# Performance work log

Measured on AMD Instinct MI355X. Metric: run time of the kernel, lower is better.

Reference implementation:

```python
import jax, jax.numpy as jnp
import numpy as np

T, K, E, H, I = 1024, 2, 8, 2048, 1024


def setup_inputs() -> dict:
    key = jax.random.key(0)
    k1, k2, k3, k4 = jax.random.split(key, 4)
    hidden_states = jax.random.normal(k1, (T, H), dtype=jnp.float32)
    selected_experts = jax.random.randint(k2, (T, K), 0, E, dtype=jnp.int32)
    # glorot-ish scale for the batched expert kernels
    gu_scale = (2.0 / (H + 2 * I)) ** 0.5
    dn_scale = (2.0 / (I + H)) ** 0.5
    gate_up_proj = jax.random.normal(k3, (E, 2 * I, H), dtype=jnp.float32) * gu_scale
    down_proj = jax.random.normal(k4, (E, H, I), dtype=jnp.float32) * dn_scale
    return {
        "hidden_states": hidden_states,
        "selected_experts": selected_experts,
        "gate_up_proj": gate_up_proj,
        "down_proj": down_proj,
    }


def reference(hidden_states, selected_experts, gate_up_proj, down_proj):
    # Mathematically identical to the original per-token weight gather
    # (ops.take + 'th,temh->tem'), but expressed as dense all-expert GEMMs
    # followed by an output gather, avoiding the T*k*2I*H weight blowup.
    # gate_up_all: (T, E, 2I)
    gate_up_all = jnp.einsum("th,emh->tem", hidden_states, gate_up_proj)
    gate, up = jnp.split(gate_up_all, 2, axis=-1)
    intermediate = jax.nn.silu(gate) * up                # (T, E, I)
    out_all = jnp.einsum("tem,ehm->teh", intermediate, down_proj)  # (T, E, H)
    # select the top-k experts' outputs per token -> (T, K, H)
    return jnp.take_along_axis(out_all, selected_experts[..., None].astype(jnp.int32), axis=1)
```

## Files before the change

kernel.cpp:

```cpp
#include <hip/hip_runtime.h>
#include <hip/hip_bf16.h>

#define T_TOK 1024
#define KSEL  2
#define NEXP  8
#define HDIM  2048
#define IDIM  1024
#define TK    (T_TOK * KSEL)

#define RS 40

typedef float  f32x4  __attribute__((ext_vector_type(4)));
typedef __bf16 bf16x8 __attribute__((ext_vector_type(8)));
typedef __bf16 bf16x2 __attribute__((ext_vector_type(2)));

__device__ __forceinline__ unsigned short f2bf(float f) {
    union { float f; unsigned u; } v; v.f = f;
    unsigned r = (v.u >> 16) & 1u;
    return (unsigned short)((v.u + 0x7fffu + r) >> 16);
}

__device__ __forceinline__ unsigned pk2bf(float lo, float hi) {
#if __has_builtin(__builtin_amdgcn_cvt_pk_bf16_f32)
    bf16x2 v = __builtin_amdgcn_cvt_pk_bf16_f32(lo, hi);
    union { bf16x2 v; unsigned u; } c; c.v = v;
    return c.u;
#else
    return (unsigned)f2bf(lo) | ((unsigned)f2bf(hi) << 16);
#endif
}

__device__ __forceinline__ void st_bf4(unsigned short* dst, float4 v) {
    uint2 u;
    u.x = pk2bf(v.x, v.y);
    u.y = pk2bf(v.z, v.w);
    *(uint2*)dst = u;
}

__global__ void build_pairs(const int* __restrict__ sel, int* __restrict__ meta,
                            int* __restrict__ pairs) {
    __shared__ int lcnt[NEXP], lstart[NEXP], lfill[NEXP];
    const int tid = threadIdx.x;
    if (tid < NEXP) { lcnt[tid] = 0; lfill[tid] = 0; }
    __syncthreads();
    for (int idx = tid; idx < TK; idx += 256) atomicAdd(&lcnt[sel[idx]], 1);
    __syncthreads();
    if (tid == 0) {
        int s = 0;
        for (int e = 0; e < NEXP; ++e) { lstart[e] = s; s += lcnt[e]; }
    }
    __syncthreads();
    for (int idx = tid; idx < TK; idx += 256) {
        int e = sel[idx];
        int pos = lstart[e] + atomicAdd(&lfill[e], 1);
        pairs[pos] = idx;
    }
    if (tid < NEXP) { meta[tid] = lcnt[tid]; meta[NEXP + tid] = lstart[tid]; }
}

__global__ __launch_bounds__(256) void gemm1_gateup(
    const float* __restrict__ hidden, const float* __restrict__ gup,
    const int* __restrict__ meta, const int* __restrict__ pairs,
    unsigned short* __restrict__ inter)
{
    __shared__ __align__(16) unsigned short As[2][64 * RS];
    __shared__ __align__(16) unsigned short Bs[2][128 * RS];

    const int bx = blockIdx.x;
    const int nt = bx & 15, e = (bx >> 4) & 7, mt = bx >> 7;
    const int cnt = meta[e];
    const int m0 = mt * 64;
    if (m0 >= cnt) return;
    const int seg  = meta[8 + e];
    const int rows = min(64, cnt - m0);
    const int n0   = nt * 64;

    const int tid  = threadIdx.x;
    const int lane = tid & 63, wave = tid >> 6;
    const int quad = lane >> 4, l16 = lane & 15;
    const int wm = wave >> 1, wn = wave & 1;

    const float* __restrict__ Wb = gup + (size_t)e * (2 * IDIM * HDIM);

    const float* aptr[2]; bool aval[2]; int aofs[2];
    #pragma unroll
    for (int c = 0; c < 2; ++c) {
        int id = tid + c * 256;
        int r = id >> 3, col = (id & 7) * 4;
        aval[c] = (r < rows);
        int tok = aval[c] ? (pairs[seg + m0 + r] >> 1) : 0;
        aptr[c] = hidden + (size_t)tok * HDIM + col;
        aofs[c] = r * RS + col;
    }
    const float* bptr[4]; int bofs[4];
    #pragma unroll
    for (int c = 0; c < 4; ++c) {
        int id = tid + c * 256;
        int r = id >> 3, col = (id & 7) * 4;
        int wr = (r < 64) ? (n0 + r) : (IDIM + n0 + (r - 64));
        bptr[c] = Wb + (size_t)wr * HDIM + col;
        bofs[c] = r * RS + col;
    }

    f32x4 accg[2][2], accu[2][2];
    const f32x4 zero = {0.f, 0.f, 0.f, 0.f};
    #pragma unroll
    for (int i = 0; i < 2; ++i)
        #pragma unroll
        for (int j = 0; j < 2; ++j) { accg[i][j] = zero; accu[i][j] = zero; }

    const float4 z4 = make_float4(0.f, 0.f, 0.f, 0.f);
    float4 Qa0[2], Qb0[4], Qa1[2], Qb1[4];

    auto load0 = [&](int k0) {
        #pragma unroll
        for (int c = 0; c < 2; ++c) Qa0[c] = aval[c] ? *(const float4*)(aptr[c] + k0) : z4;
        #pragma unroll
        for (int c = 0; c < 4; ++c) Qb0[c] = *(const float4*)(bptr[c] + k0);
    };
    auto load1 = [&](int k0) {
        #pragma unroll
        for (int c = 0; c < 2; ++c) Qa1[c] = aval[c] ? *(const float4*)(aptr[c] + k0) : z4;
        #pragma unroll
        for (int c = 0; c < 4; ++c) Qb1[c] = *(const float4*)(bptr[c] + k0);
    };
    auto store0 = [&](int buf) {
        #pragma unroll
        for (int c = 0; c < 2; ++c) st_bf4(&As[buf][aofs[c]], Qa0[c]);
        #pragma unroll
        for (int c = 0; c < 4; ++c) st_bf4(&Bs[buf][bofs[c]], Qb0[c]);
    };
    auto store1 = [&](int buf) {
        #pragma unroll
        for (int c = 0; c < 2; ++c) st_bf4(&As[buf][aofs[c]], Qa1[c]);
        #pragma unroll
        for (int c = 0; c < 4; ++c) st_bf4(&Bs[buf][bofs[c]], Qb1[c]);
    };
    auto compute = [&](int buf) {
        bf16x8 af[2], bg[2], bu[2];
        const int kq = quad * 8;
        #pragma unroll
        for (int i = 0; i < 2; ++i)
            af[i] = *(const bf16x8*)&As[buf][(wm * 32 + i * 16 + l16) * RS + kq];
        #pragma unroll
        for (int j = 0; j < 2; ++j) {
            bg[j] = *(const bf16x8*)&Bs[buf][(wn * 32 + j * 16 + l16) * RS + kq];
            bu[j] = *(const bf16x8*)&Bs[buf][(64 + wn * 32 + j * 16 + l16) * RS + kq];
        }
        #pragma unroll
        for (int i = 0; i < 2; ++i)
            #pragma unroll
            for (int j = 0; j < 2; ++j) {
                accg[i][j] = __builtin_amdgcn_mfma_f32_16x16x32_bf16(af[i], bg[j], accg[i][j], 0, 0, 0);
                accu[i][j] = __builtin_amdgcn_mfma_f32_16x16x32_bf16(af[i], bu[j], accu[i][j], 0, 0, 0);
            }
    };

    const int NK = HDIM / 32;
    load0(0);
    store0(0);
    load1(32);
    load0(64);
    __syncthreads();

    for (int k = 0; ; k += 2) {
        compute(0);
        store1(1);
        if (k + 3 < NK) load1((k + 3) * 32);
        __syncthreads();
        compute(1);
        if (k + 2 >= NK) break;
        store0(0);
        if (k + 4 < NK) load0((k + 4) * 32);
        __syncthreads();
    }

    #pragma unroll
    for (int i = 0; i < 2; ++i) {
        #pragma unroll
        for (int r = 0; r < 4; ++r) {
            int ml = wm * 32 + i * 16 + quad * 4 + r;
            if (ml < rows) {
                size_t orow = (size_t)(seg + m0 + ml) * IDIM;
                #pragma unroll
                for (int j = 0; j < 2; ++j) {
                    int n = n0 + wn * 32 + j * 16 + l16;
                    float g = accg[i][j][r], u = accu[i][j][r];
                    float s = g * (1.f / (1.f + __expf(-g)));
                    inter[orow + n] = f2bf(s * u);
                }
            }
        }
    }
}

__global__ __launch_bounds__(256, 4) void gemm2_down(
    const unsigned short* __restrict__ inter, const float* __restrict__ down,
    const int* __restrict__ meta, const int* __restrict__ pairs,
    float* __restrict__ out)
{
    __shared__ __align__(16) unsigned short As[2][64 * RS];
    __shared__ __align__(16) unsigned short Bs[2][64 * RS];

    const int bx = blockIdx.x;
    const int nt = bx & 31, e = (bx >> 5) & 7, mt = bx >> 8;
    const int cnt = meta[e];
    const int m0 = mt * 64;
    if (m0 >= cnt) return;
    const int seg  = meta[8 + e];
    const int rows = min(64, cnt - m0);
    const int n0   = nt * 64;

    const int tid  = threadIdx.x;
    const int lane = tid & 63, wave = tid >> 6;
    const int quad = lane >> 4, l16 = lane & 15;
    const int wm = wave >> 1, wn = wave & 1;

    const float* __restrict__ Db = down + (size_t)e * (HDIM * IDIM);

    const int ar = tid >> 2, ako = (tid & 3) * 8;
    const bool aval = (ar < rows);
    const unsigned short* iptr = inter + (size_t)(seg + m0 + (aval ? ar : 0)) * IDIM + ako;
    const int aofs = ar * RS + ako;

    const float* bptr[2]; int bofs[2];
    #pragma unroll
    for (int c = 0; c < 2; ++c) {
        int id = tid + c * 256;
        int r = id >> 3, col = (id & 7) * 4;
        bptr[c] = Db + (size_t)(n0 + r) * IDIM + col;
        bofs[c] = r * RS + col;
    }

    f32x4 acc[2][2];
    const f32x4 zero = {0.f, 0.f, 0.f, 0.f};
    #pragma unroll
    for (int i = 0; i < 2; ++i)
        #pragma unroll
        for (int j = 0; j < 2; ++j) acc[i][j] = zero;

    const uint4 zu4 = make_uint4(0u, 0u, 0u, 0u);
    uint4 QaU0, QaU1; float4 Qb0[2], Qb1[2];

    auto load0 = [&](int k0) {
        QaU0 = aval ? *(const uint4*)(iptr + k0) : zu4;
        #pragma unroll
        for (int c = 0; c < 2; ++c) Qb0[c] = *(const float4*)(bptr[c] + k0);
    };
    auto load1 = [&](int k0) {
        QaU1 = aval ? *(const uint4*)(iptr + k0) : zu4;
        #pragma unroll
        for (int c = 0; c < 2; ++c) Qb1[c] = *(const float4*)(bptr[c] + k0);
    };
    auto store0 = [&](int buf) {
        *(uint4*)&As[buf][aofs] = QaU0;
        #pragma unroll
        for (int c = 0; c < 2; ++c) st_bf4(&Bs[buf][bofs[c]], Qb0[c]);
    };
    auto store1 = [&](int buf) {
        *(uint4*)&As[buf][aofs] = QaU1;
        #pragma unroll
        for (int c = 0; c < 2; ++c) st_bf4(&Bs[buf][bofs[c]], Qb1[c]);
    };
    auto compute = [&](int buf) {
        bf16x8 af[2], bf[2];
        const int kq = quad * 8;
        #pragma unroll
        for (int i = 0; i < 2; ++i)
            af[i] = *(const bf16x8*)&As[buf][(wm * 32 + i * 16 + l16) * RS + kq];
        #pragma unroll
        for (int j = 0; j < 2; ++j)
            bf[j] = *(const bf16x8*)&Bs[buf][(wn * 32 + j * 16 + l16) * RS + kq];
        #pragma unroll
        for (int i = 0; i < 2; ++i)
            #pragma unroll
            for (int j = 0; j < 2; ++j)
                acc[i][j] = __builtin_amdgcn_mfma_f32_16x16x32_bf16(af[i], bf[j], acc[i][j], 0, 0, 0);
    };

    const int NK = IDIM / 32;
    load0(0);
    store0(0);
    load1(32);
    load0(64);
    __syncthreads();

    for (int k = 0; ; k += 2) {
        compute(0);
        store1(1);
        if (k + 3 < NK) load1((k + 3) * 32);
        __syncthreads();
        compute(1);
        if (k + 2 >= NK) break;
        store0(0);
        if (k + 4 < NK) load0((k + 4) * 32);
        __syncthreads();
    }

    #pragma unroll
    for (int i = 0; i < 2; ++i) {
        #pragma unroll
        for (int r = 0; r < 4; ++r) {
            int ml = wm * 32 + i * 16 + quad * 4 + r;
            if (ml < rows) {
                int p = pairs[seg + m0 + ml];
                size_t ob = (size_t)p * HDIM + n0 + wn * 32 + l16;
                #pragma unroll
                for (int j = 0; j < 2; ++j)
                    out[ob + j * 16] = acc[i][j][r];
            }
        }
    }
}

extern "C" void kernel_launch(void* const* d_in, const int* in_sizes, int n_in,
                              void* d_out, int out_size, void* d_ws, size_t ws_size,
                              hipStream_t stream) {
    const float* hidden = (const float*)d_in[0];
    const int*   sel    = (const int*)  d_in[1];
    const float* gup    = (const float*)d_in[2];
    const float* down   = (const float*)d_in[3];
    float* out = (float*)d_out;

    int* meta  = (int*)d_ws;
    int* pairs = meta + 16;
    unsigned short* inter = (unsigned short*)((char*)d_ws + 16384);

    build_pairs<<<1, 256, 0, stream>>>(sel, meta, pairs);
    gemm1_gateup<<<4096, 256, 0, stream>>>(hidden, gup, meta, pairs, inter);
    gemm2_down  <<<8192, 256, 0, stream>>>(inter, down, meta, pairs, out);
}
```

Measured before the change: 339.0 us.

## Pre-convert weights and activations to bf16 and widen K tile to 64

```diff
diff --git a/kernel.cpp b/kernel.cpp
--- a/kernel.cpp
+++ b/kernel.cpp
@@ -8,7 +8,8 @@
 #define IDIM  1024
 #define TK    (T_TOK * KSEL)
 
-#define RS 40
+#define BK 64
+#define RS 72
 
 typedef float  f32x4  __attribute__((ext_vector_type(4)));
 typedef __bf16 bf16x8 __attribute__((ext_vector_type(8)));
@@ -30,13 +31,6 @@
 #endif
 }
 
-__device__ __forceinline__ void st_bf4(unsigned short* dst, float4 v) {
-    uint2 u;
-    u.x = pk2bf(v.x, v.y);
-    u.y = pk2bf(v.z, v.w);
-    *(uint2*)dst = u;
-}
-
 __global__ void build_pairs(const int* __restrict__ sel, int* __restrict__ meta,
                             int* __restrict__ pairs) {
     __shared__ int lcnt[NEXP], lstart[NEXP], lfill[NEXP];
@@ -58,16 +52,159 @@
     if (tid < NEXP) { meta[tid] = lcnt[tid]; meta[NEXP + tid] = lstart[tid]; }
 }
 
-__global__ __launch_bounds__(256) void gemm1_gateup(
-    const float* __restrict__ hidden, const float* __restrict__ gup,
+__global__ __launch_bounds__(256) void cvt_all(
+    const float* __restrict__ gup, const float* __restrict__ down,
+    const float* __restrict__ hidden, unsigned short* __restrict__ gup_bf,
+    unsigned short* __restrict__ down_bf, unsigned short* __restrict__ hid_bf)
+{
+    const long NG = (long)NEXP * 2 * IDIM * HDIM / 8;
+    const long ND = (long)NEXP * HDIM * IDIM / 8;
+    const long NH = (long)T_TOK * HDIM / 8;
+    const long NT = NG + ND + NH;
+    for (long i = (long)blockIdx.x * 256 + threadIdx.x; i < NT;
+         i += (long)gridDim.x * 256) {
+        const float* s; unsigned short* d; long c;
+        if (i < NG)           { s = gup;    d = gup_bf;  c = i; }
+        else if (i < NG + ND) { s = down;   d = down_bf; c = i - NG; }
+        else                  { s = hidden; d = hid_bf;  c = i - NG - ND; }
+        float4 v0 = *(const float4*)(s + c * 8);
+        float4 v1 = *(const float4*)(s + c * 8 + 4);
+        uint4 o;
+        o.x = pk2bf(v0.x, v0.y); o.y = pk2bf(v0.z, v0.w);
+        o.z = pk2bf(v1.x, v1.y); o.w = pk2bf(v1.z, v1.w);
+        *(uint4*)(d + c * 8) = o;
+    }
+}
+
+__global__ __launch_bounds__(256, 4) void gemm1_gateup(
+    const unsigned short* __restrict__ hid_bf, const unsigned short* __restrict__ gup_bf,
     const int* __restrict__ meta, const int* __restrict__ pairs,
     unsigned short* __restrict__ inter)
 {
     __shared__ __align__(16) unsigned short As[2][64 * RS];
-    __shared__ __align__(16) unsigned short Bs[2][128 * RS];
+    __shared__ __align__(16) unsigned short Bs[2][64 * RS];
 
     const int bx = blockIdx.x;
-    const int nt = bx & 15, e = (bx >> 4) & 7, mt = bx >> 7;
+    const int e = bx & 7, mt = (bx >> 3) & 31, nt = bx >> 8;
+    const int cnt = meta[e];
+    const int m0 = mt * 64;
+    if (m0 >= cnt) return;
+    const int seg  = meta[8 + e];
+    const int rows = min(64, cnt - m0);
+    const int n0   = nt * 32;
+
+    const int tid  = threadIdx.x;
+    const int lane = tid & 63, wave = tid >> 6;
+    const int quad = lane >> 4, l16 = lane & 15;
+    const int wm = wave >> 1, wn = wave & 1;
+
+    const unsigned short* __restrict__ Wb = gup_bf + (size_t)e * (2 * IDIM * HDIM);
+
+    const unsigned short* aptr[2]; int aofs[2];
+    #pragma unroll
+    for (int c = 0; c < 2; ++c) {
+        int id = tid + c * 256;
+        int row = id >> 3, kc = (id & 7) * 8;
+        int ar = min(row, rows - 1);
+        int tok = pairs[seg + m0 + ar] >> 1;
+        aptr[c] = hid_bf + (size_t)tok * HDIM + kc;
+        aofs[c] = row * RS + kc;
+    }
+    const unsigned short* bptr[2]; int bofs[2];
+    #pragma unroll
+    for (int c = 0; c < 2; ++c) {
+        int id = tid + c * 256;
+        int row = id >> 3, kc = (id & 7) * 8;
+        int gr = (row < 32) ? (n0 + row) : (IDIM + n0 + (row - 32));
+        bptr[c] = Wb + (size_t)gr * HDIM + kc;
+        bofs[c] = row * RS + kc;
+    }
+
+    f32x4 accg[2], accu[2];
+    const f32x4 zero = {0.f, 0.f, 0.f, 0.f};
+    accg[0] = zero; accg[1] = zero; accu[0] = zero; accu[1] = zero;
+
+    uint4 Qa0[2], Qb0[2], Qa1[2], Qb1[2];
+    auto load0 = [&](int k0) {
+        #pragma unroll
+        for (int c = 0; c < 2; ++c) { Qa0[c] = *(const uint4*)(aptr[c] + k0);
+                                      Qb0[c] = *(const uint4*)(bptr[c] + k0); }
+    };
+    auto load1 = [&](int k0) {
+        #pragma unroll
+        for (int c = 0; c < 2; ++c) { Qa1[c] = *(const uint4*)(aptr[c] + k0);
+                                      Qb1[c] = *(const uint4*)(bptr[c] + k0); }
+    };
+    auto store0 = [&](int buf) {
+        #pragma unroll
+        for (int c = 0; c < 2; ++c) { *(uint4*)&As[buf][aofs[c]] = Qa0[c];
+                                      *(uint4*)&Bs[buf][bofs[c]] = Qb0[c]; }
+    };
+    auto store1 = [&](int buf) {
+        #pragma unroll
+        for (int c = 0; c < 2; ++c) { *(uint4*)&As[buf][aofs[c]] = Qa1[c];
+                                      *(uint4*)&Bs[buf][bofs[c]] = Qb1[c]; }
+    };
+    auto compute = [&](int buf) {
+        #pragma unroll
+        for (int ks = 0; ks < 2; ++ks) {
+            const int kq = ks * 32 + quad * 8;
+            bf16x8 af0 = *(const bf16x8*)&As[buf][(wm * 32 + l16) * RS + kq];
+            bf16x8 af1 = *(const bf16x8*)&As[buf][(wm * 32 + 16 + l16) * RS + kq];
+            bf16x8 bg  = *(const bf16x8*)&Bs[buf][(wn * 16 + l16) * RS + kq];
+            bf16x8 bu  = *(const bf16x8*)&Bs[buf][(32 + wn * 16 + l16) * RS + kq];
+            accg[0] = __builtin_amdgcn_mfma_f32_16x16x32_bf16(af0, bg, accg[0], 0, 0, 0);
+            accg[1] = __builtin_amdgcn_mfma_f32_16x16x32_bf16(af1, bg, accg[1], 0, 0, 0);
+            accu[0] = __builtin_amdgcn_mfma_f32_16x16x32_bf16(af0, bu, accu[0], 0, 0, 0);
+            accu[1] = __builtin_amdgcn_mfma_f32_16x16x32_bf16(af1, bu, accu[1], 0, 0, 0);
+        }
+    };
+
+    const int NK = HDIM / BK;
+    load0(0);
+    store0(0);
+    load1(BK);
+    load0(2 * BK);
+    __syncthreads();
+    for (int k = 0; ; k += 2) {
+        compute(0);
+        store1(1);
+        if (k + 3 < NK) load1((k + 3) * BK);
+        __syncthreads();
+        compute(1);
+        if (k + 2 >= NK) break;
+        store0(0);
+        if (k + 4 < NK) load0((k + 4) * BK);
+        __syncthreads();
+    }
+
+    #pragma unroll
+    for (int i = 0; i < 2; ++i) {
+        #pragma unroll
+        for (int r = 0; r < 4; ++r) {
+            int ml = wm * 32 + i * 16 + quad * 4 + r;
+            if (ml < rows) {
+                size_t orow = (size_t)(seg + m0 + ml) * IDIM;
+                int n = n0 + wn * 16 + l16;
+                float g = (i == 0) ? accg[0][r] : accg[1][r];
+                float u = (i == 0) ? accu[0][r] : accu[1][r];
+                float s = g * (1.f / (1.f + __expf(-g)));
+                inter[orow + n] = f2bf(s * u);
+            }
+        }
+    }
+}
+
+__global__ __launch_bounds__(256, 4) void gemm2_down(
+    const unsigned short* __restrict__ inter, const unsigned short* __restrict__ down_bf,
+    const int* __restrict__ meta, const int* __restrict__ pairs,
+    float* __restrict__ out)
+{
+    __shared__ __align__(16) unsigned short As[2][64 * RS];
+    __shared__ __align__(16) unsigned short Bs[2][64 * RS];
+
+    const int bx = blockIdx.x;
+    const int e = bx & 7, mt = (bx >> 3) & 31, nt = bx >> 8;
     const int cnt = meta[e];
     const int m0 = mt * 64;
     if (m0 >= cnt) return;
@@ -80,220 +217,81 @@
     const int quad = lane >> 4, l16 = lane & 15;
     const int wm = wave >> 1, wn = wave & 1;
 
-    const float* __restrict__ Wb = gup + (size_t)e * (2 * IDIM * HDIM);
-
-    const float* aptr[2]; bool aval[2]; int aofs[2];
+    const unsigned short* __restrict__ Db = down_bf + (size_t)e * (HDIM * IDIM);
+
+    const unsigned short* aptr[2]; int aofs[2];
     #pragma unroll
     for (int c = 0; c < 2; ++c) {
         int id = tid + c * 256;
-        int r = id >> 3, col = (id & 7) * 4;
-        aval[c] = (r < rows);
-        int tok = aval[c] ? (pairs[seg + m0 + r] >> 1) : 0;
-        aptr[c] = hidden + (size_t)tok * HDIM + col;
-        aofs[c] = r * RS + col;
-    }
-    const float* bptr[4]; int bofs[4];
-    #pragma unroll
-    for (int c = 0; c < 4; ++c) {
+        int row = id >> 3, kc = (id & 7) * 8;
+        int ar = min(row, rows - 1);
+        aptr[c] = inter + (size_t)(seg + m0 + ar) * IDIM + kc;
+        aofs[c] = row * RS + kc;
+    }
+    const unsigned short* bptr[2]; int bofs[2];
+    #pragma unroll
+    for (int c = 0; c < 2; ++c) {
         int id = tid + c * 256;
-        int r = id >> 3, col = (id & 7) * 4;
-        int wr = (r < 64) ? (n0 + r) : (IDIM + n0 + (r - 64));
-        bptr[c] = Wb + (size_t)wr * HDIM + col;
-        bofs[c] = r * RS + col;
-    }
-
-    f32x4 accg[2][2], accu[2][2];
+        int row = id >> 3, kc = (id & 7) * 8;
+        bptr[c] = Db + (size_t)(n0 + row) * IDIM + kc;
+        bofs[c] = row * RS + kc;
+    }
+
+    f32x4 acc[2][2];
     const f32x4 zero = {0.f, 0.f, 0.f, 0.f};
-    #pragma unroll
-    for (int i = 0; i < 2; ++i)
-        #pragma unroll
-        for (int j = 0; j < 2; ++j) { accg[i][j] = zero; accu[i][j] = zero; }
-
-    const float4 z4 = make_float4(0.f, 0.f, 0.f, 0.f);
-    float4 Qa0[2], Qb0[4], Qa1[2], Qb1[4];
-
+    acc[0][0] = zero; acc[0][1] = zero; acc[1][0] = zero; acc[1][1] = zero;
+
+    uint4 Qa0[2], Qb0[2], Qa1[2], Qb1[2];
     auto load0 = [&](int k0) {
         #pragma unroll
-        for (int c = 0; c < 2; ++c) Qa0[c] = aval[c] ? *(const float4*)(aptr[c] + k0) : z4;
-        #pragma unroll
-        for (int c = 0; c < 4; ++c) Qb0[c] = *(const float4*)(bptr[c] + k0);
+        for (int c = 0; c < 2; ++c) { Qa0[c] = *(const uint4*)(aptr[c] + k0);
+                                      Qb0[c] = *(const uint4*)(bptr[c] + k0); }
     };
     auto load1 = [&](int k0) {
         #pragma unroll
-        for (int c = 0; c < 2; ++c) Qa1[c] = aval[c] ? *(const float4*)(aptr[c] + k0) : z4;
-        #pragma unroll
-        for (int c = 0; c < 4; ++c) Qb1[c] = *(const float4*)(bptr[c] + k0);
+        for (int c = 0; c < 2; ++c) { Qa1[c] = *(const uint4*)(aptr[c] + k0);
+                                      Qb1[c] = *(const uint4*)(bptr[c] + k0); }
     };
     auto store0 = [&](int buf) {
         #pragma unroll
-        for (int c = 0; c < 2; ++c) st_bf4(&As[buf][aofs[c]], Qa0[c]);
-        #pragma unroll
-        for (int c = 0; c < 4; ++c) st_bf4(&Bs[buf][bofs[c]], Qb0[c]);
+        for (int c = 0; c < 2; ++c) { *(uint4*)&As[buf][aofs[c]] = Qa0[c];
+                                      *(uint4*)&Bs[buf][bofs[c]] = Qb0[c]; }
     };
     auto store1 = [&](int buf) {
         #pragma unroll
-        for (int c = 0; c < 2; ++c) st_bf4(&As[buf][aofs[c]], Qa1[c]);
-        #pragma unroll
-        for (int c = 0; c < 4; ++c) st_bf4(&Bs[buf][bofs[c]], Qb1[c]);
+        for (int c = 0; c < 2; ++c) { *(uint4*)&As[buf][aofs[c]] = Qa1[c];
+                                      *(uint4*)&Bs[buf][bofs[c]] = Qb1[c]; }
     };
     auto compute = [&](int buf) {
-        bf16x8 af[2], bg[2], bu[2];
-        const int kq = quad * 8;
-        #pragma unroll
-        for (int i = 0; i < 2; ++i)
-            af[i] = *(const bf16x8*)&As[buf][(wm * 32 + i * 16 + l16) * RS + kq];
-        #pragma unroll
-        for (int j = 0; j < 2; ++j) {
-            bg[j] = *(const bf16x8*)&Bs[buf][(wn * 32 + j * 16 + l16) * RS + kq];
-            bu[j] = *(const bf16x8*)&Bs[buf][(64 + wn * 32 + j * 16 + l16) * RS + kq];
+        #pragma unroll
+        for (int ks = 0; ks < 2; ++ks) {
+            const int kq = ks * 32 + quad * 8;
+            bf16x8 af0 = *(const bf16x8*)&As[buf][(wm * 32 + l16) * RS + kq];
+            bf16x8 af1 = *(const bf16x8*)&As[buf][(wm * 32 + 16 + l16) * RS + kq];
+            bf16x8 bf0 = *(const bf16x8*)&Bs[buf][(wn * 32 + l16) * RS + kq];
+            bf16x8 bf1 = *(const bf16x8*)&Bs[buf][(wn * 32 + 16 + l16) * RS + kq];
+            acc[0][0] = __builtin_amdgcn_mfma_f32_16x16x32_bf16(af0, bf0, acc[0][0], 0, 0, 0);
+            acc[0][1] = __builtin_amdgcn_mfma_f32_16x16x32_bf16(af0, bf1, acc[0][1], 0, 0, 0);
+            acc[1][0] = __builtin_amdgcn_mfma_f32_16x16x32_bf16(af1, bf0, acc[1][0], 0, 0, 0);
+            acc[1][1] = __builtin_amdgcn_mfma_f32_16x16x32_bf16(af1, bf1, acc[1][1], 0, 0, 0);
         }
-        #pragma unroll
-        for (int i = 0; i < 2; ++i)
-            #pragma unroll
-            for (int j = 0; j < 2; ++j) {
-                accg[i][j] = __builtin_amdgcn_mfma_f32_16x16x32_bf16(af[i], bg[j], accg[i][j], 0, 0, 0);
-                accu[i][j] = __builtin_amdgcn_mfma_f32_16x16x32_bf16(af[i], bu[j], accu[i][j], 0, 0, 0);
-            }
-    };
-
-    const int NK = HDIM / 32;
+    };
+
+    const int NK = IDIM / BK;
     load0(0);
     store0(0);
-    load1(32);
-    load0(64);
-    __syncthreads();
-
+    load1(BK);
+    load0(2 * BK);
+    __syncthreads();
     for (int k = 0; ; k += 2) {
         compute(0);
         store1(1);
-        if (k + 3 < NK) load1((k + 3) * 32);
+        if (k + 3 < NK) load1((k + 3) * BK);
         __syncthreads();
         compute(1);
         if (k + 2 >= NK) break;
         store0(0);
-        if (k + 4 < NK) load0((k + 4) * 32);
-        __syncthreads();
-    }
-
-    #pragma unroll
-    for (int i = 0; i < 2; ++i) {
-        #pragma unroll
-        for (int r = 0; r < 4; ++r) {
-            int ml = wm * 32 + i * 16 + quad * 4 + r;
-            if (ml < rows) {
-                size_t orow = (size_t)(seg + m0 + ml) * IDIM;
-                #pragma unroll
-                for (int j = 0; j < 2; ++j) {
-                    int n = n0 + wn * 32 + j * 16 + l16;
-                    float g = accg[i][j][r], u = accu[i][j][r];
-                    float s = g * (1.f / (1.f + __expf(-g)));
-                    inter[orow + n] = f2bf(s * u);
-                }
-            }
-        }
-    }
-}
-
-__global__ __launch_bounds__(256, 4) void gemm2_down(
-    const unsigned short* __restrict__ inter, const float* __restrict__ down,
-    const int* __restrict__ meta, const int* __restrict__ pairs,
-    float* __restrict__ out)
-{
-    __shared__ __align__(16) unsigned short As[2][64 * RS];
-    __shared__ __align__(16) unsigned short Bs[2][64 * RS];
-
-    const int bx = blockIdx.x;
-    const int nt = bx & 31, e = (bx >> 5) & 7, mt = bx >> 8;
-    const int cnt = meta[e];
-    const int m0 = mt * 64;
-    if (m0 >= cnt) return;
-    const int seg  = meta[8 + e];
-    const int rows = min(64, cnt - m0);
-    const int n0   = nt * 64;
-
-    const int tid  = threadIdx.x;
-    const int lane = tid & 63, wave = tid >> 6;
-    const int quad = lane >> 4, l16 = lane & 15;
-    const int wm = wave >> 1, wn = wave & 1;
-
-    const float* __restrict__ Db = down + (size_t)e * (HDIM * IDIM);
-
-    const int ar = tid >> 2, ako = (tid & 3) * 8;
-    const bool aval = (ar < rows);
-    const unsigned short* iptr = inter + (size_t)(seg + m0 + (aval ? ar : 0)) * IDIM + ako;
-    const int aofs = ar * RS + ako;
-
-    const float* bptr[2]; int bofs[2];
-    #pragma unroll
-    for (int c = 0; c < 2; ++c) {
-        int id = tid + c * 256;
-        int r = id >> 3, col = (id & 7) * 4;
-        bptr[c] = Db + (size_t)(n0 + r) * IDIM + col;
-        bofs[c] = r * RS + col;
-    }
-
-    f32x4 acc[2][2];
-    const f32x4 zero = {0.f, 0.f, 0.f, 0.f};
-    #pragma unroll
-    for (int i = 0; i < 2; ++i)
-        #pragma unroll
-        for (int j = 0; j < 2; ++j) acc[i][j] = zero;
-
-    const uint4 zu4 = make_uint4(0u, 0u, 0u, 0u);
-    uint4 QaU0, QaU1; float4 Qb0[2], Qb1[2];
-
-    auto load0 = [&](int k0) {
-        QaU0 = aval ? *(const uint4*)(iptr + k0) : zu4;
-        #pragma unroll
-        for (int c = 0; c < 2; ++c) Qb0[c] = *(const float4*)(bptr[c] + k0);
-    };
-    auto load1 = [&](int k0) {
-        QaU1 = aval ? *(const uint4*)(iptr + k0) : zu4;
-        #pragma unroll
-        for (int c = 0; c < 2; ++c) Qb1[c] = *(const float4*)(bptr[c] + k0);
-    };
-    auto store0 = [&](int buf) {
-        *(uint4*)&As[buf][aofs] = QaU0;
-        #pragma unroll
-        for (int c = 0; c < 2; ++c) st_bf4(&Bs[buf][bofs[c]], Qb0[c]);
-    };
-    auto store1 = [&](int buf) {
-        *(uint4*)&As[buf][aofs] = QaU1;
-        #pragma unroll
-        for (int c = 0; c < 2; ++c) st_bf4(&Bs[buf][bofs[c]], Qb1[c]);
-    };
-    auto compute = [&](int buf) {
-        bf16x8 af[2], bf[2];
-        const int kq = quad * 8;
-        #pragma unroll
-        for (int i = 0; i < 2; ++i)
-            af[i] = *(const bf16x8*)&As[buf][(wm * 32 + i * 16 + l16) * RS + kq];
-        #pragma unroll
-        for (int j = 0; j < 2; ++j)
-            bf[j] = *(const bf16x8*)&Bs[buf][(wn * 32 + j * 16 + l16) * RS + kq];
-        #pragma unroll
-        for (int i = 0; i < 2; ++i)
-            #pragma unroll
-            for (int j = 0; j < 2; ++j)
-                acc[i][j] = __builtin_amdgcn_mfma_f32_16x16x32_bf16(af[i], bf[j], acc[i][j], 0, 0, 0);
-    };
-
-    const int NK = IDIM / 32;
-    load0(0);
-    store0(0);
-    load1(32);
-    load0(64);
-    __syncthreads();
-
-    for (int k = 0; ; k += 2) {
-        compute(0);
-        store1(1);
-        if (k + 3 < NK) load1((k + 3) * 32);
-        __syncthreads();
-        compute(1);
-        if (k + 2 >= NK) break;
-        store0(0);
-        if (k + 4 < NK) load0((k + 4) * 32);
+        if (k + 4 < NK) load0((k + 4) * BK);
         __syncthreads();
     }
 
@@ -305,9 +303,8 @@
             if (ml < rows) {
                 int p = pairs[seg + m0 + ml];
                 size_t ob = (size_t)p * HDIM + n0 + wn * 32 + l16;
-                #pragma unroll
-                for (int j = 0; j < 2; ++j)
-                    out[ob + j * 16] = acc[i][j][r];
+                out[ob]      = acc[i][0][r];
+                out[ob + 16] = acc[i][1][r];
             }
         }
     }
@@ -322,11 +319,16 @@
     const float* down   = (const float*)d_in[3];
     float* out = (float*)d_out;
 
-    int* meta  = (int*)d_ws;
+    char* ws = (char*)d_ws;
+    int* meta  = (int*)ws;
     int* pairs = meta + 16;
-    unsigned short* inter = (unsigned short*)((char*)d_ws + 16384);
+    unsigned short* inter   = (unsigned short*)(ws + 16384);
+    unsigned short* gup_bf  = inter + (size_t)TK * IDIM;
+    unsigned short* down_bf = gup_bf + (size_t)NEXP * 2 * IDIM * HDIM;
+    unsigned short* hid_bf  = down_bf + (size_t)NEXP * HDIM * IDIM;
 
     build_pairs<<<1, 256, 0, stream>>>(sel, meta, pairs);
-    gemm1_gateup<<<4096, 256, 0, stream>>>(hidden, gup, meta, pairs, inter);
-    gemm2_down  <<<8192, 256, 0, stream>>>(inter, down, meta, pairs, out);
-}
+    cvt_all<<<6400, 256, 0, stream>>>(gup, down, hidden, gup_bf, down_bf, hid_bf);
+    gemm1_gateup<<<8192, 256, 0, stream>>>(hid_bf, gup_bf, meta, pairs, inter);
+    gemm2_down  <<<8192, 256, 0, stream>>>(inter, down_bf, meta, pairs, out);
+}
```

After: 706.4 us. 108% more time.
